# Kernel optimization log

Hardware: AMD Instinct MI355X
Metric: run time of the kernel (lower is better)

Reference implementation:

```python
import jax, jax.numpy as jnp
import numpy as np

EPS = 1e-5
NEG_SLOPE = 0.01  # torch LeakyReLU default

def setup_inputs() -> dict:
    N, D, T, H = 4096, 64, 60, 128
    key = jax.random.key(0)
    ks = jax.random.split(key, 12)
    s_ih = 1.0 / np.sqrt(H)
    return {
        "x": jax.random.normal(ks[0], (N, D, T), dtype=jnp.float32),
        "bn1_gamma": jnp.ones((D,), jnp.float32),
        "bn1_beta": jnp.zeros((D,), jnp.float32),
        "W_ih": jax.random.uniform(ks[1], (4 * H, D), jnp.float32, -s_ih, s_ih),
        "W_hh": jax.random.uniform(ks[2], (4 * H, H), jnp.float32, -s_ih, s_ih),
        "b_ih": jax.random.uniform(ks[3], (4 * H,), jnp.float32, -s_ih, s_ih),
        "b_hh": jax.random.uniform(ks[4], (4 * H,), jnp.float32, -s_ih, s_ih),
        "bn2_gamma": jnp.ones((H,), jnp.float32),
        "bn2_beta": jnp.zeros((H,), jnp.float32),
        "W_t": jax.random.uniform(ks[5], (H, H), jnp.float32, -s_ih, s_ih),
        "b_t": jax.random.uniform(ks[6], (H,), jnp.float32, -s_ih, s_ih),
        "a": jax.random.normal(ks[7], (2 * H, 1), dtype=jnp.float32),
        "W_fc": jax.random.uniform(ks[8], (H, H), jnp.float32, -s_ih, s_ih),
        "b_fc": jax.random.uniform(ks[9], (H,), jnp.float32, -s_ih, s_ih),
        "W_out": jax.random.uniform(ks[10], (1, H), jnp.float32, -s_ih, s_ih),
        "b_out": jax.random.uniform(ks[11], (1,), jnp.float32, -s_ih, s_ih),
    }

def _leaky(z):
    return jnp.where(z >= 0, z, NEG_SLOPE * z)

def _lstm_last(x, W_ih, W_hh, b_ih, b_hh):
    # x: [N, T, D] -> last hidden state [N, H]
    N, T, D = x.shape
    H = W_hh.shape[1]
    # precompute input contributions for all timesteps: [T, N, 4H]
    xg = jnp.einsum('ntd,gd->tng', x, W_ih) + b_ih + b_hh
    h0 = jnp.zeros((N, H), x.dtype)
    c0 = jnp.zeros((N, H), x.dtype)
    def step(carry, g):
        h, c = carry
        gates = g + h @ W_hh.T
        i, f, gg, o = jnp.split(gates, 4, axis=-1)
        i = jax.nn.sigmoid(i)
        f = jax.nn.sigmoid(f)
        gg = jnp.tanh(gg)
        o = jax.nn.sigmoid(o)
        c = f * c + i * gg
        h = o * jnp.tanh(c)
        return (h, c), None
    (h, _), _ = jax.lax.scan(step, (h0, c0), xg)
    return h

def reference(x, bn1_gamma, bn1_beta, W_ih, W_hh, b_ih, b_hh,
              bn2_gamma, bn2_beta, W_t, b_t, a, W_fc, b_fc, W_out, b_out):
    # BatchNorm1d over channels of [N, D, T] (training-mode batch stats)
    m1 = x.mean(axis=(0, 2), keepdims=True)
    v1 = x.var(axis=(0, 2), keepdims=True)
    xn = (x - m1) * jax.lax.rsqrt(v1 + EPS)
    xn = xn * bn1_gamma[None, :, None] + bn1_beta[None, :, None]
    xs = jnp.transpose(xn, (0, 2, 1))  # [N, T, D]
    hidden = _lstm_last(xs, W_ih, W_hh, b_ih, b_hh)  # [N, H]
    # BatchNorm1d on [N, H]
    m2 = hidden.mean(axis=0, keepdims=True)
    v2 = hidden.var(axis=0, keepdims=True)
    hidden = (hidden - m2) * jax.lax.rsqrt(v2 + EPS) * bn2_gamma + bn2_beta
    # attention: scores[i,j] = a1.t[j] + a2.t[i]  (decomposed, no NxNx2H concat)
    H = hidden.shape[1]
    t = hidden @ W_t.T + b_t  # [N, H]
    s1 = t @ a[:H, 0]   # contribution of column node j
    s2 = t @ a[H:, 0]   # contribution of row node i
    scores = _leaky(s2[:, None] + s1[None, :])  # [N, N]
    att = jax.nn.softmax(scores, axis=1)
    h2 = att @ hidden + hidden
    h3 = _leaky(h2 @ W_fc.T + b_fc)
    out = jax.nn.sigmoid(h3 @ W_out.T + b_out)  # [N, 1]
    return out.squeeze(-1)
```

## Files before the change

### kernel.cpp

```cpp
#include <hip/hip_runtime.h>
#include <math.h>

constexpr int NN = 4096, DD = 64, TT = 60, HH = 128, GG = 512, KK = 192;

typedef _Float16 h8 __attribute__((ext_vector_type(8)));
typedef float f4 __attribute__((ext_vector_type(4)));

constexpr size_t XNT = 0;
constexpr size_t WFRG = (size_t)TT * NN * DD / 2;
constexpr size_t BSUM = WFRG + 98304 / 2;
constexpr size_t SC1 = BSUM + GG;
constexpr size_t SH1 = SC1 + DD;
constexpr size_t HID = SH1 + DD;
constexpr size_t HBN = HID + (size_t)NN * HH;
constexpr size_t SC2 = HBN + (size_t)NN * HH;
constexpr size_t SH2 = SC2 + HH;
constexpr size_t U1O = SH2 + HH;
constexpr size_t U2O = U1O + HH;
constexpr size_t CCO = U2O + HH;
constexpr size_t S1O = CCO + 4;
constexpr size_t S2O = S1O + NN;
constexpr size_t H2O = S2O + NN;
constexpr size_t SSUM = H2O + (size_t)NN * HH;
constexpr size_t SC16 = SSUM + 392;

__device__ __forceinline__ float fastrcp_(float x) { return __builtin_amdgcn_rcpf(x); }
__device__ __forceinline__ float sigmoidf_(float x) { return fastrcp_(1.f + __expf(-x)); }
__device__ __forceinline__ float tanhfast_(float x) { return 1.f - 2.f * fastrcp_(__expf(2.f * x) + 1.f); }
__device__ __forceinline__ float leakyf_(float z) { return fmaxf(z, 0.01f * z); }

__device__ __forceinline__ unsigned fenc_(float f) {
    unsigned b = __float_as_uint(f);
    return (b & 0x80000000u) ? ~b : (b | 0x80000000u);
}
__device__ __forceinline__ float fdec_(unsigned u) {
    return (u & 0x80000000u) ? __uint_as_float(u & 0x7fffffffu) : __uint_as_float(~u);
}

constexpr int TSTR = 264;

__global__ __launch_bounds__(256) void k_pre(const float* __restrict__ x,
                                             const float* __restrict__ g1,
                                             const float* __restrict__ b1,
                                             const float* __restrict__ Wih,
                                             const float* __restrict__ Whh,
                                             const float* __restrict__ bih,
                                             const float* __restrict__ bhh,
                                             const float* __restrict__ Wt,
                                             const float* __restrict__ bt,
                                             const float* __restrict__ a,
                                             float* __restrict__ ws) {
    int b = blockIdx.x;
    int tid = threadIdx.x;
    if (b >= 1024) {
        if (b == 1408) {
            int k = tid;
            if (k < HH) {
                float u1 = 0.f, u2 = 0.f;
                for (int j = 0; j < HH; j++) {
                    float w = Wt[j * HH + k];
                    u1 = fmaf(w, a[j], u1);
                    u2 = fmaf(w, a[HH + j], u2);
                }
                ws[U1O + k] = u1;
                ws[U2O + k] = u2;
                if (k == 0) {
                    float c1 = 0.f, c2 = 0.f;
                    for (int j = 0; j < HH; j++) {
                        c1 = fmaf(bt[j], a[j], c1);
                        c2 = fmaf(bt[j], a[HH + j], c2);
                    }
                    ws[CCO] = c1;
                    ws[CCO + 1] = c2;
                    ((unsigned*)ws)[CCO + 2] = fenc_(-1e30f);
                }
            }
            return;
        }
        int o = (b - 1024) * 256 + tid;
        _Float16* wf = (_Float16*)(ws + WFRG);
        int j = o & 7;
        int lane = (o >> 3) & 63;
        int rest = o >> 9;
        int ks = rest % 6;
        int gw = rest / 6;
        int g = gw & 3, w = gw >> 2;
        int col = g * 128 + w * 16 + (lane & 15);
        int k = ks * 32 + (lane >> 4) * 8 + j;
        float v = (k < DD) ? Wih[col * DD + k] : Whh[col * HH + (k - DD)];
        wf[o] = (_Float16)v;
        return;
    }
    __shared__ _Float16 stg[TT * TSTR];
    __shared__ float rs[256], rss[256];
    __shared__ float scs[64], shs[64];
    __shared__ unsigned done;
    const float4* xb = (const float4*)(x + (size_t)b * 15360);
#pragma unroll
    for (int q = 0; q < 15; q++) {
        int f = q * 256 + tid;
        float4 v = xb[f];
        int k = f / 15, t0 = (f - k * 15) * 4;
        stg[(t0 + 0) * TSTR + k] = (_Float16)v.x;
        stg[(t0 + 1) * TSTR + k] = (_Float16)v.y;
        stg[(t0 + 2) * TSTR + k] = (_Float16)v.z;
        stg[(t0 + 3) * TSTR + k] = (_Float16)v.w;
    }
    __syncthreads();
    {
        int k = tid;
        float s = 0.f, ss = 0.f;
#pragma unroll
        for (int t = 0; t < TT; t++) {
            float v = (float)stg[t * TSTR + k];
            s += v;
            ss = fmaf(v, v, ss);
        }
        rs[tid] = s; rss[tid] = ss;
    }
    __syncthreads();
    if (tid < 64) {
        float ts = rs[tid] + rs[64 + tid] + rs[128 + tid] + rs[192 + tid];
        float tss = rss[tid] + rss[64 + tid] + rss[128 + tid] + rss[192 + tid];
        atomicAdd(&ws[SSUM + tid], ts);
        atomicAdd(&ws[SSUM + 64 + tid], tss);
    }
    __syncthreads();
    if (tid == 0) {
        __threadfence();
        done = atomicAdd((unsigned*)(ws + SSUM) + 128, 1u);
    }
    __syncthreads();
    _Float16* outp = (_Float16*)ws;
    int n0 = b * 4;
    for (int p = tid; p < 3840; p += 256) {
        int t = p >> 6, i = p & 63;
        *(uint2*)(outp + ((size_t)t * NN + n0) * DD + i * 4) =
            *(const uint2*)(stg + t * TSTR + i * 4);
    }
    if (done != 1023u) return;
    __threadfence();
    if (tid < 64) {
        float cnt = (float)(NN * TT);
        float m = ws[SSUM + tid] / cnt;
        float var = ws[SSUM + 64 + tid] / cnt - m * m;
        float sc = g1[tid] * rsqrtf(var + 1e-5f);
        scs[tid] = sc;
        shs[tid] = b1[tid] - m * sc;
        ((_Float16*)(ws + SC16))[tid] = (_Float16)sc;
    }
    __syncthreads();
    for (int c = tid; c < GG; c += 256) {
        float bsum = bih[c] + bhh[c];
        const float4* wr = (const float4*)(Wih + c * 64);
#pragma unroll
        for (int q = 0; q < 16; q++) {
            float4 wv = wr[q];
            bsum = fmaf(wv.x, shs[q * 4], fmaf(wv.y, shs[q * 4 + 1],
                   fmaf(wv.z, shs[q * 4 + 2], fmaf(wv.w, shs[q * 4 + 3], bsum))));
        }
        ws[BSUM + c] = bsum;
    }
}

__global__ __launch_bounds__(512, 1) void k_lstm(const float* __restrict__ g2,
                                                 const float* __restrict__ b2,
                                                 float* __restrict__ ws) {
    int tid = threadIdx.x;
    int w = tid >> 6, lane = tid & 63;
    int quad = lane >> 4, m = lane & 15;
    int r0 = blockIdx.x * 16;
    __shared__ _Float16 hlds[2][16][136];
    __shared__ unsigned dn;
    const _Float16* wf = (const _Float16*)(ws + WFRG);

    h8 bw[4][6];
#pragma unroll
    for (int g = 0; g < 4; g++)
#pragma unroll
        for (int ks = 0; ks < 6; ks++)
            bw[g][ks] = *(const h8*)(wf + ((((w * 4 + g) * 6 + ks) * 64 + lane) * 8));

    float bias[4];
#pragma unroll
    for (int g = 0; g < 4; g++) bias[g] = ws[BSUM + g * 128 + w * 16 + m];

    const _Float16* sc16 = (const _Float16*)(ws + SC16);
    h8 scv0 = *(const h8*)(sc16 + quad * 8);
    h8 scv1 = *(const h8*)(sc16 + 32 + quad * 8);

    for (int p = tid; p < 2 * 16 * 136; p += 512) ((_Float16*)hlds)[p] = (_Float16)0.f;

    f4 cst = {};
    float hv[4];
    const _Float16* xb = (const _Float16*)ws + (size_t)(r0 + m) * DD + quad * 8;
    __syncthreads();

    h8 ax0 = (*(const h8*)xb) * scv0;
    h8 ax1 = (*(const h8*)(xb + 32)) * scv1;

    for (int t = 0; t < TT; t++) {
        h8 ah[4];
        const _Float16* hb = &hlds[(t + 1) & 1][m][quad * 8];
#pragma unroll
        for (int ks = 0; ks < 4; ks++) ah[ks] = *(const h8*)(hb + ks * 32);
        h8 nx0 = {}, nx1 = {};
        if (t + 1 < TT) {
            const _Float16* xp = xb + (size_t)(t + 1) * NN * DD;
            nx0 = *(const h8*)xp;
            nx1 = *(const h8*)(xp + 32);
        }

        f4 acc[4];
#pragma unroll
        for (int g = 0; g < 4; g++) acc[g] = (f4){bias[g], bias[g], bias[g], bias[g]};
#pragma unroll
        for (int g = 0; g < 4; g++) acc[g] = __builtin_amdgcn_mfma_f32_16x16x32_f16(ax0, bw[g][0], acc[g], 0, 0, 0);
#pragma unroll
        for (int g = 0; g < 4; g++) acc[g] = __builtin_amdgcn_mfma_f32_16x16x32_f16(ax1, bw[g][1], acc[g], 0, 0, 0);
#pragma unroll
        for (int ks = 0; ks < 4; ks++)
#pragma unroll
            for (int g = 0; g < 4; g++)
                acc[g] = __builtin_amdgcn_mfma_f32_16x16x32_f16(ah[ks], bw[g][ks + 2], acc[g], 0, 0, 0);

#pragma unroll
        for (int r = 0; r < 4; r++) {
            float ig = sigmoidf_(acc[0][r]);
            float fg = sigmoidf_(acc[1][r]);
            float gg = tanhfast_(acc[2][r]);
            float og = sigmoidf_(acc[3][r]);
            float c = fmaf(fg, cst[r], ig * gg);
            cst[r] = c;
            hv[r] = og * tanhfast_(c);
        }
        _Float16* wbuf = &hlds[t & 1][0][0];
        int col = w * 16 + m;
#pragma unroll
        for (int r = 0; r < 4; r++) wbuf[(quad * 4 + r) * 136 + col] = (_Float16)hv[r];
        __syncthreads();
        ax0 = nx0 * scv0;
        ax1 = nx1 * scv1;
    }
    int col = w * 16 + m;
#pragma unroll
    for (int r = 0; r < 4; r++)
        ws[HID + (size_t)(r0 + quad * 4 + r) * HH + col] = hv[r];

    float s = hv[0] + hv[1] + hv[2] + hv[3];
    float ss = fmaf(hv[0], hv[0], fmaf(hv[1], hv[1], fmaf(hv[2], hv[2], hv[3] * hv[3])));
    s += __shfl_xor(s, 16, 64); s += __shfl_xor(s, 32, 64);
    ss += __shfl_xor(ss, 16, 64); ss += __shfl_xor(ss, 32, 64);
    if (quad == 0) {
        atomicAdd(&ws[SSUM + 132 + col], s);
        atomicAdd(&ws[SSUM + 260 + col], ss);
    }
    __syncthreads();
    if (tid == 0) {
        __threadfence();
        dn = atomicAdd((unsigned*)(ws + SSUM) + 129, 1u);
    }
    __syncthreads();
    if (dn == 255u) {
        __threadfence();
        if (tid < 128) {
            float mm = ws[SSUM + 132 + tid] / (float)NN;
            float var = ws[SSUM + 260 + tid] / (float)NN - mm * mm;
            float sc = g2[tid] * rsqrtf(var + 1e-5f);
            ws[SC2 + tid] = sc;
            ws[SH2 + tid] = b2[tid] - mm * sc;
        }
    }
}

__global__ void k_hbn(float* __restrict__ ws) {
    __shared__ float sc[HH], sh[HH], u1s[HH], u2s[HH];
    __shared__ _Float16 swz[4096];
    int tid = threadIdx.x;
    if (tid < HH) {
        sc[tid] = ws[SC2 + tid]; sh[tid] = ws[SH2 + tid];
        u1s[tid] = ws[U1O + tid]; u2s[tid] = ws[U2O + tid];
    }
    __syncthreads();
    int r = tid >> 3, l = tid & 7;
    int n = blockIdx.x * 32 + r;
    const float* hr = ws + HID + (size_t)n * HH;
    float* hb = ws + HBN + (size_t)n * HH;
    int lanehi = (r >> 3);
    int jj = r & 7;
    float d1 = 0.f, d2 = 0.f;
    int k0 = l * 16;
#pragma unroll
    for (int q4 = 0; q4 < 4; q4++) {
        float4 hv4 = *(const float4*)&hr[k0 + q4 * 4];
        float4 o;
#pragma unroll
        for (int c = 0; c < 4; c++) {
            int kk = k0 + q4 * 4 + c;
            float v = fmaf(((const float*)&hv4)[c], sc[kk], sh[kk]);
            ((float*)&o)[c] = v;
            swz[l * 512 + (lanehi * 16 + (kk & 15)) * 8 + jj] = (_Float16)v;
            d1 = fmaf(v, u1s[kk], d1);
            d2 = fmaf(v, u2s[kk], d2);
        }
        *(float4*)&hb[k0 + q4 * 4] = o;
    }
#pragma unroll
    for (int o = 1; o < 8; o <<= 1) { d1 += __shfl_xor(d1, o, 64); d2 += __shfl_xor(d2, o, 64); }
    if (l == 0) {
        float s1 = d1 + ws[CCO];
        ws[S1O + n] = s1;
        ws[S2O + n] = d2 + ws[CCO + 1];
        atomicMax((unsigned*)ws + CCO + 2, fenc_(s1));
    }
    __syncthreads();
    _Float16* dst = (_Float16*)ws + (size_t)blockIdx.x * 4096;
    for (int p = tid; p < 512; p += 256)
        *(h8*)(dst + p * 8) = *(const h8*)(swz + p * 8);
}

__global__ __launch_bounds__(512, 1) void k_attfc(const float* __restrict__ Wfc,
                                                  const float* __restrict__ bfc,
                                                  const float* __restrict__ Wout,
                                                  const float* __restrict__ bout,
                                                  float* __restrict__ ws,
                                                  float* __restrict__ out) {
    __shared__ float ls1[NN];
    __shared__ float red[4][16][132];
    __shared__ float psr[4][16];
    __shared__ float h2s[16][132];
    int tid = threadIdx.x;
    int w = tid >> 6, lane = tid & 63;
    int quad = lane >> 4, m = lane & 15;
    int whalf = w >> 2, jsplit = w & 3;
    int n0 = blockIdx.x * 16;
    for (int i = tid; i < NN; i += 512) ls1[i] = ws[S1O + i];
    __syncthreads();
    float s1max = fdec_(((unsigned*)ws)[CCO + 2]);
    float s2n = ws[S2O + n0 + m];
    float mi = leakyf_(s2n + s1max);
    const _Float16* hbsw = (const _Float16*)ws;
    f4 acc[4] = {};
    float psum = 0.f;
    for (int jt0 = 0; jt0 < 32; jt0++) {
        int jt = jsplit * 32 + jt0;
        const float* sp = &ls1[jt * 32 + quad * 8];
        h8 ap;
        float ps = 0.f;
#pragma unroll
        for (int jj = 0; jj < 8; jj++) {
            float z = s2n + sp[jj];
            float p = __expf(leakyf_(z) - mi);
            ps += p;
            ap[jj] = (_Float16)p;
        }
        psum += ps;
#pragma unroll
        for (int hgi = 0; hgi < 4; hgi++) {
            int hg = whalf * 4 + hgi;
            h8 bb = *(const h8*)(hbsw + ((size_t)(jt * 8 + hg) * 64 + lane) * 8);
            acc[hgi] = __builtin_amdgcn_mfma_f32_16x16x32_f16(ap, bb, acc[hgi], 0, 0, 0);
        }
    }
    psum += __shfl_xor(psum, 16, 64);
    psum += __shfl_xor(psum, 32, 64);
    if (whalf == 0 && lane < 16) psr[jsplit][lane] = psum;
#pragma unroll
    for (int hgi = 0; hgi < 4; hgi++) {
        int h = (whalf * 4 + hgi) * 16 + m;
#pragma unroll
        for (int r = 0; r < 4; r++)
            red[jsplit][quad * 4 + r][h] = acc[hgi][r];
    }
    __syncthreads();
    if (tid < 16) {
        float pt = psr[0][tid] + psr[1][tid] + psr[2][tid] + psr[3][tid];
        psr[0][tid] = fastrcp_(pt);
    }
    __syncthreads();
#pragma unroll
    for (int cc = 0; cc < 4; cc++) {
        int c = cc * 512 + tid;
        int row = c >> 7, h = c & 127;
        float v = red[0][row][h] + red[1][row][h] + red[2][row][h] + red[3][row][h];
        h2s[row][h] = fmaf(v, psr[0][row], ws[HBN + (size_t)(n0 + row) * HH + h]);
    }
    __syncthreads();
    int row = tid >> 5, jj = tid & 31;
    float po = 0.f;
#pragma unroll
    for (int q = 0; q < 4; q++) {
        int j = q * 32 + jj;
        const float4* wr = (const float4*)(Wfc + (size_t)j * HH);
        float a = 0.f;
#pragma unroll 8
        for (int kq = 0; kq < 32; kq++) {
            float4 wv = wr[kq];
            float4 hv = *(const float4*)&h2s[row][kq * 4];
            a = fmaf(wv.x, hv.x, fmaf(wv.y, hv.y, fmaf(wv.z, hv.z, fmaf(wv.w, hv.w, a))));
        }
        po = fmaf(leakyf_(a + bfc[j]), Wout[j], po);
    }
#pragma unroll
    for (int o = 1; o < 32; o <<= 1) po += __shfl_xor(po, o, 64);
    if (jj == 0) out[n0 + row] = fastrcp_(1.f + __expf(-(po + bout[0])));
}

extern "C" void kernel_launch(void* const* d_in, const int* in_sizes, int n_in,
                              void* d_out, int out_size, void* d_ws, size_t ws_size,
                              hipStream_t stream) {
    const float* x = (const float*)d_in[0];
    const float* bn1_g = (const float*)d_in[1];
    const float* bn1_b = (const float*)d_in[2];
    const float* W_ih = (const float*)d_in[3];
    const float* W_hh = (const float*)d_in[4];
    const float* b_ih = (const float*)d_in[5];
    const float* b_hh = (const float*)d_in[6];
    const float* bn2_g = (const float*)d_in[7];
    const float* bn2_b = (const float*)d_in[8];
    const float* W_t = (const float*)d_in[9];
    const float* b_t = (const float*)d_in[10];
    const float* a = (const float*)d_in[11];
    const float* W_fc = (const float*)d_in[12];
    const float* b_fc = (const float*)d_in[13];
    const float* W_out = (const float*)d_in[14];
    const float* b_out = (const float*)d_in[15];
    float* ws = (float*)d_ws;
    float* out = (float*)d_out;

    hipMemsetAsync((char*)d_ws + SSUM * sizeof(float), 0, 392 * sizeof(float), stream);
    k_pre<<<1409, 256, 0, stream>>>(x, bn1_g, bn1_b, W_ih, W_hh, b_ih, b_hh, W_t, b_t, a, ws);
    k_lstm<<<NN / 16, 512, 0, stream>>>(bn2_g, bn2_b, ws);
    k_hbn<<<NN / 32, 256, 0, stream>>>(ws);
    k_attfc<<<NN / 16, 512, 0, stream>>>(W_fc, b_fc, W_out, b_out, ws, out);
}
```

Baseline: 295.6 us.

## Split LSTM gate GEMM K-dimension across two wave halves with LDS reduction

Doubles the LSTM block to 1024 threads: one half of the waves computes the input and first hidden slice contributions, the other half the remaining hidden slices, and partial gate sums are exchanged through shared memory. Each half then applies the gate nonlinearities for two of the four rows. This shortens the per-timestep serial MFMA chain and halves per-wave elementwise work, at the cost of an extra block barrier and LDS traffic each step and higher thread count per CU.

```diff
diff --git a/kernel.cpp b/kernel.cpp
--- a/kernel.cpp
+++ b/kernel.cpp
@@ -163,92 +163,127 @@
     }
 }
 
-__global__ __launch_bounds__(512, 1) void k_lstm(const float* __restrict__ g2,
-                                                 const float* __restrict__ b2,
-                                                 float* __restrict__ ws) {
+__global__ __launch_bounds__(1024, 1) void k_lstm(const float* __restrict__ g2,
+                                                  const float* __restrict__ b2,
+                                                  float* __restrict__ ws) {
     int tid = threadIdx.x;
     int w = tid >> 6, lane = tid & 63;
     int quad = lane >> 4, m = lane & 15;
+    int p = w & 7, half = w >> 3;
+    int base = half * 2;
+    int col = p * 16 + m;
     int r0 = blockIdx.x * 16;
     __shared__ _Float16 hlds[2][16][136];
+    __shared__ f4 xch[16][2][64];
     __shared__ unsigned dn;
     const _Float16* wf = (const _Float16*)(ws + WFRG);
 
-    h8 bw[4][6];
+    h8 bw[4][3];
 #pragma unroll
     for (int g = 0; g < 4; g++)
 #pragma unroll
-        for (int ks = 0; ks < 6; ks++)
-            bw[g][ks] = *(const h8*)(wf + ((((w * 4 + g) * 6 + ks) * 64 + lane) * 8));
+        for (int ks = 0; ks < 3; ks++)
+            bw[g][ks] = *(const h8*)(wf + ((((p * 4 + g) * 6 + (half * 3 + ks)) * 64 + lane) * 8));
 
     float bias[4];
 #pragma unroll
-    for (int g = 0; g < 4; g++) bias[g] = ws[BSUM + g * 128 + w * 16 + m];
+    for (int g = 0; g < 4; g++) bias[g] = half ? ws[BSUM + g * 128 + col] : 0.f;
 
     const _Float16* sc16 = (const _Float16*)(ws + SC16);
     h8 scv0 = *(const h8*)(sc16 + quad * 8);
     h8 scv1 = *(const h8*)(sc16 + 32 + quad * 8);
 
-    for (int p = tid; p < 2 * 16 * 136; p += 512) ((_Float16*)hlds)[p] = (_Float16)0.f;
-
-    f4 cst = {};
-    float hv[4];
+    for (int q = tid; q < 2 * 16 * 136; q += 1024) ((_Float16*)hlds)[q] = (_Float16)0.f;
+
+    float cst[2] = {0.f, 0.f};
+    float hvv[2];
     const _Float16* xb = (const _Float16*)ws + (size_t)(r0 + m) * DD + quad * 8;
     __syncthreads();
 
-    h8 ax0 = (*(const h8*)xb) * scv0;
-    h8 ax1 = (*(const h8*)(xb + 32)) * scv1;
+    h8 ax0 = {}, ax1 = {};
+    if (half == 0) {
+        ax0 = (*(const h8*)xb) * scv0;
+        ax1 = (*(const h8*)(xb + 32)) * scv1;
+    }
 
     for (int t = 0; t < TT; t++) {
-        h8 ah[4];
+        f4 acc[4];
+        h8 nx0 = {}, nx1 = {};
         const _Float16* hb = &hlds[(t + 1) & 1][m][quad * 8];
-#pragma unroll
-        for (int ks = 0; ks < 4; ks++) ah[ks] = *(const h8*)(hb + ks * 32);
-        h8 nx0 = {}, nx1 = {};
-        if (t + 1 < TT) {
-            const _Float16* xp = xb + (size_t)(t + 1) * NN * DD;
-            nx0 = *(const h8*)xp;
-            nx1 = *(const h8*)(xp + 32);
-        }
-
-        f4 acc[4];
-#pragma unroll
-        for (int g = 0; g < 4; g++) acc[g] = (f4){bias[g], bias[g], bias[g], bias[g]};
-#pragma unroll
-        for (int g = 0; g < 4; g++) acc[g] = __builtin_amdgcn_mfma_f32_16x16x32_f16(ax0, bw[g][0], acc[g], 0, 0, 0);
-#pragma unroll
-        for (int g = 0; g < 4; g++) acc[g] = __builtin_amdgcn_mfma_f32_16x16x32_f16(ax1, bw[g][1], acc[g], 0, 0, 0);
-#pragma unroll
-        for (int ks = 0; ks < 4; ks++)
-#pragma unroll
-            for (int g = 0; g < 4; g++)
-                acc[g] = __builtin_amdgcn_mfma_f32_16x16x32_f16(ah[ks], bw[g][ks + 2], acc[g], 0, 0, 0);
-
-#pragma unroll
-        for (int r = 0; r < 4; r++) {
-            float ig = sigmoidf_(acc[0][r]);
-            float fg = sigmoidf_(acc[1][r]);
-            float gg = tanhfast_(acc[2][r]);
-            float og = sigmoidf_(acc[3][r]);
-            float c = fmaf(fg, cst[r], ig * gg);
-            cst[r] = c;
-            hv[r] = og * tanhfast_(c);
+        if (half == 0) {
+            h8 ah0 = *(const h8*)hb;
+            if (t + 1 < TT) {
+                const _Float16* xp = xb + (size_t)(t + 1) * NN * DD;
+                nx0 = *(const h8*)xp;
+                nx1 = *(const h8*)(xp + 32);
+            }
+#pragma unroll
+            for (int g = 0; g < 4; g++) acc[g] = (f4){0.f, 0.f, 0.f, 0.f};
+#pragma unroll
+            for (int g = 0; g < 4; g++) acc[g] = __builtin_amdgcn_mfma_f32_16x16x32_f16(ax0, bw[g][0], acc[g], 0, 0, 0);
+#pragma unroll
+            for (int g = 0; g < 4; g++) acc[g] = __builtin_amdgcn_mfma_f32_16x16x32_f16(ax1, bw[g][1], acc[g], 0, 0, 0);
+#pragma unroll
+            for (int g = 0; g < 4; g++) acc[g] = __builtin_amdgcn_mfma_f32_16x16x32_f16(ah0, bw[g][2], acc[g], 0, 0, 0);
+        } else {
+            h8 ah1 = *(const h8*)(hb + 32);
+            h8 ah2 = *(const h8*)(hb + 64);
+            h8 ah3 = *(const h8*)(hb + 96);
+#pragma unroll
+            for (int g = 0; g < 4; g++) acc[g] = (f4){bias[g], bias[g], bias[g], bias[g]};
+#pragma unroll
+            for (int g = 0; g < 4; g++) acc[g] = __builtin_amdgcn_mfma_f32_16x16x32_f16(ah1, bw[g][0], acc[g], 0, 0, 0);
+#pragma unroll
+            for (int g = 0; g < 4; g++) acc[g] = __builtin_amdgcn_mfma_f32_16x16x32_f16(ah2, bw[g][1], acc[g], 0, 0, 0);
+#pragma unroll
+            for (int g = 0; g < 4; g++) acc[g] = __builtin_amdgcn_mfma_f32_16x16x32_f16(ah3, bw[g][2], acc[g], 0, 0, 0);
+        }
+        f4 s0, s1;
+        if (half == 0) {
+            s0 = (f4){acc[0][2], acc[1][2], acc[2][2], acc[3][2]};
+            s1 = (f4){acc[0][3], acc[1][3], acc[2][3], acc[3][3]};
+        } else {
+            s0 = (f4){acc[0][0], acc[1][0], acc[2][0], acc[3][0]};
+            s1 = (f4){acc[0][1], acc[1][1], acc[2][1], acc[3][1]};
+        }
+        xch[w][0][lane] = s0;
+        xch[w][1][lane] = s1;
+        __syncthreads();
+        f4 in0 = xch[w ^ 8][0][lane];
+        f4 in1 = xch[w ^ 8][1][lane];
+#pragma unroll
+        for (int rr = 0; rr < 2; rr++) {
+            f4 inn = rr ? in1 : in0;
+            f4 own;
+            if (half == 0)
+                own = rr ? (f4){acc[0][1], acc[1][1], acc[2][1], acc[3][1]}
+                         : (f4){acc[0][0], acc[1][0], acc[2][0], acc[3][0]};
+            else
+                own = rr ? (f4){acc[0][3], acc[1][3], acc[2][3], acc[3][3]}
+                         : (f4){acc[0][2], acc[1][2], acc[2][2], acc[3][2]};
+            float ig = sigmoidf_(own[0] + inn[0]);
+            float fg = sigmoidf_(own[1] + inn[1]);
+            float gg = tanhfast_(own[2] + inn[2]);
+            float og = sigmoidf_(own[3] + inn[3]);
+            float c = fmaf(fg, cst[rr], ig * gg);
+            cst[rr] = c;
+            hvv[rr] = og * tanhfast_(c);
         }
         _Float16* wbuf = &hlds[t & 1][0][0];
-        int col = w * 16 + m;
-#pragma unroll
-        for (int r = 0; r < 4; r++) wbuf[(quad * 4 + r) * 136 + col] = (_Float16)hv[r];
+#pragma unroll
+        for (int rr = 0; rr < 2; rr++) wbuf[(quad * 4 + base + rr) * 136 + col] = (_Float16)hvv[rr];
+        if (half == 0) {
+            ax0 = nx0 * scv0;
+            ax1 = nx1 * scv1;
+        }
         __syncthreads();
-        ax0 = nx0 * scv0;
-        ax1 = nx1 * scv1;
-    }
-    int col = w * 16 + m;
-#pragma unroll
-    for (int r = 0; r < 4; r++)
-        ws[HID + (size_t)(r0 + quad * 4 + r) * HH + col] = hv[r];
-
-    float s = hv[0] + hv[1] + hv[2] + hv[3];
-    float ss = fmaf(hv[0], hv[0], fmaf(hv[1], hv[1], fmaf(hv[2], hv[2], hv[3] * hv[3])));
+    }
+#pragma unroll
+    for (int rr = 0; rr < 2; rr++)
+        ws[HID + (size_t)(r0 + quad * 4 + base + rr) * HH + col] = hvv[rr];
+
+    float s = hvv[0] + hvv[1];
+    float ss = fmaf(hvv[0], hvv[0], hvv[1] * hvv[1]);
     s += __shfl_xor(s, 16, 64); s += __shfl_xor(s, 32, 64);
     ss += __shfl_xor(ss, 16, 64); ss += __shfl_xor(ss, 32, 64);
     if (quad == 0) {
@@ -430,7 +465,7 @@
 
     hipMemsetAsync((char*)d_ws + SSUM * sizeof(float), 0, 392 * sizeof(float), stream);
     k_pre<<<1409, 256, 0, stream>>>(x, bn1_g, bn1_b, W_ih, W_hh, b_ih, b_hh, W_t, b_t, a, ws);
-    k_lstm<<<NN / 16, 512, 0, stream>>>(bn2_g, bn2_b, ws);
+    k_lstm<<<NN / 16, 1024, 0, stream>>>(bn2_g, bn2_b, ws);
     k_hbn<<<NN / 32, 256, 0, stream>>>(ws);
     k_attfc<<<NN / 16, 512, 0, stream>>>(W_fc, b_fc, W_out, b_out, ws, out);
 }
```

New measurement: 324.3 us. 1.1x slower.
